# Kernel tuning notes

Hardware: AMD Instinct MI355X
Metric: run time of the kernel (lower is better)

## Reference

```python
import jax, jax.numpy as jnp
import numpy as np

MARGIN = 0.2
ALPHA = 2.0
BETA = 1.5
ANGLE_THRESHOLD = 30.0
EPS_PD = 1e-6   # F.pairwise_distance eps
EPS_CS = 1e-8   # F.cosine_similarity eps
NEG_INF = -1e30
POS_INF = 1e30


def setup_inputs() -> dict:
    key = jax.random.key(0)
    k1, k2, k3 = jax.random.split(key, 3)
    B, F, A = 4096, 512, 3
    features = jax.random.normal(k1, (B, F), dtype=jnp.float32)
    labels = jax.random.randint(k2, (B,), 0, 256)
    angles = jax.random.uniform(k3, (B, A), dtype=jnp.float32) * 90.0  # degrees
    features_orig = jax.random.normal(jax.random.fold_in(key, 7), (B, F), dtype=jnp.float32)
    return {"features": features, "labels": labels, "angles": angles, "features_orig": features_orig}


def _cosine_sim_matrix(f):
    norms = jnp.linalg.norm(f, axis=1)
    denom = jnp.maximum(norms[:, None] * norms[None, :], EPS_CS)
    return (f @ f.T) / denom


def _forward(features, labels, angles, features_orig):
    B = features.shape[0]
    idx = jnp.arange(B)
    # pairwise angle distances [B,B] (torch.cdist p=2)
    adist = jnp.sqrt(jnp.sum((angles[:, None, :] - angles[None, :, :]) ** 2, axis=-1))
    same = labels[:, None] == labels[None, :]
    same = same & ~jnp.eye(B, dtype=bool)          # exclude self
    diff = labels[:, None] != labels[None, :]
    has_pos = same.any(axis=1)
    has_neg = diff.any(axis=1)
    valid = has_pos & has_neg
    # hardest positive: same label, largest angle difference
    pos_idx = jnp.argmax(jnp.where(same, adist, NEG_INF), axis=1)
    # hardest negative: among diff-label within angle threshold, most similar feature;
    # else diff-label with smallest angle difference
    sim = _cosine_sim_matrix(features)
    similar = diff & (adist < ANGLE_THRESHOLD)
    sim_any = similar.any(axis=1)
    neg_idx_hard = jnp.argmax(jnp.where(similar, sim, NEG_INF), axis=1)
    neg_idx_far = jnp.argmin(jnp.where(diff, adist, POS_INF), axis=1)
    neg_idx = jnp.where(sim_any, neg_idx_hard, neg_idx_far)
    # triplet distances (F.pairwise_distance adds eps to the diff)
    a = features
    p = features[pos_idx]
    n = features[neg_idx]
    pos_d = jnp.linalg.norm(a - p + EPS_PD, axis=1)
    neg_d = jnp.linalg.norm(a - n + EPS_PD, axis=1)
    # angle-based weights (non-differentiable, matches .item() in torch)
    pa = adist[idx, pos_idx]
    na = adist[idx, neg_idx]
    w = jnp.where(pa > 45.0, ALPHA, 1.0) * jnp.where(na < 15.0, BETA, 1.0)
    basic = jax.nn.relu(pos_d - neg_d + MARGIN)
    vmask = valid.astype(features.dtype)
    cnt = jnp.maximum(vmask.sum(), 1.0)
    triplet_loss = jnp.sum(w * basic * vmask) / cnt
    # reconstruction term
    num = jnp.sum(features * features_orig, axis=1)
    den = jnp.maximum(jnp.linalg.norm(features, axis=1) * jnp.linalg.norm(features_orig, axis=1), EPS_CS)
    recon = 1.0 - jnp.mean(num / den)
    return triplet_loss + 0.1 * recon


def reference(features, labels, angles, features_orig):
    return _forward(features, labels, angles, features_orig)
```

## Files before the change

kernel.cpp:

```cpp
#include <hip/hip_runtime.h>
#include <math.h>

#define BN 4096
#define FD 512
#define TT 128
#define BK 64
#define NJT (BN / TT)
#define NBLK (NJT * (NJT + 1) / 2)
#define NPC 64

typedef __attribute__((ext_vector_type(8))) __bf16 bf16x8;
typedef __attribute__((ext_vector_type(4))) float floatx4;
typedef unsigned long long u64;

__device__ __forceinline__ float wred_sum(float v) {
#pragma unroll
  for (int m = 1; m < 64; m <<= 1) v += __shfl_xor(v, m, 64);
  return v;
}

__device__ __forceinline__ float dot4(float4 a, float4 b) {
  return a.x * b.x + a.y * b.y + a.z * b.z + a.w * b.w;
}

__device__ __forceinline__ unsigned short f2bf(float x) {
  unsigned u = __float_as_uint(x);
  u += 0x7fffu + ((u >> 16) & 1u);
  return (unsigned short)(u >> 16);
}

__device__ __forceinline__ void load16(const void* g, void* l) {
  __builtin_amdgcn_global_load_lds(
      (const __attribute__((address_space(1))) unsigned int*)g,
      (__attribute__((address_space(3))) unsigned int*)l, 16, 0, 0);
}

__device__ __forceinline__ unsigned ford(float v) {
  unsigned u = __float_as_uint(v);
  return u ^ (((unsigned)((int)u >> 31)) | 0x80000000u);
}

template <int N>
__device__ __forceinline__ int rori(int x) {
  return __builtin_amdgcn_update_dpp(0, x, 0x120 | N, 0xf, 0xf, true);
}
template <int N>
__device__ __forceinline__ u64 ror16_u64(u64 k) {
  unsigned lo = (unsigned)rori<N>((int)(unsigned)k);
  unsigned hi = (unsigned)rori<N>((int)(unsigned)(k >> 32));
  return ((u64)hi << 32) | lo;
}
__device__ __forceinline__ u64 red16_max_u64(u64 k) {
  u64 o;
  o = ror16_u64<1>(k); k = o > k ? o : k;
  o = ror16_u64<2>(k); k = o > k ? o : k;
  o = ror16_u64<4>(k); k = o > k ? o : k;
  o = ror16_u64<8>(k); k = o > k ? o : k;
  return k;
}

__device__ __forceinline__ u64 sx64(u64 v, int m) {
  unsigned lo = (unsigned)__shfl_xor((int)(unsigned)v, m, 64);
  unsigned hi = (unsigned)__shfl_xor((int)(unsigned)(v >> 32), m, 64);
  return ((u64)hi << 32) | lo;
}

__global__ __launch_bounds__(256) void k_prep(const float* __restrict__ f,
                                              const float* __restrict__ fo,
                                              const float* __restrict__ angles,
                                              unsigned short* __restrict__ gb,
                                              float* __restrict__ rowr,
                                              float* __restrict__ ax,
                                              float* __restrict__ ay,
                                              float* __restrict__ az) {
  const int i = blockIdx.x * 4 + (threadIdx.x >> 6);
  const int lane = threadIdx.x & 63;
  const int t = blockIdx.x * 256 + threadIdx.x;
  if (t < BN) {
    ax[t] = angles[t * 3 + 0];
    ay[t] = angles[t * 3 + 1];
    az[t] = angles[t * 3 + 2];
  }
  const float4* fr = (const float4*)(f + (size_t)i * FD);
  const float4* orr = (const float4*)(fo + (size_t)i * FD);
  float4 x0 = fr[lane], x1 = fr[lane + 64];
  float4 y0 = orr[lane], y1 = orr[lane + 64];
  float sff = dot4(x0, x0) + dot4(x1, x1);
  float sfo = dot4(x0, y0) + dot4(x1, y1);
  float soo = dot4(y0, y0) + dot4(y1, y1);
  sff = wred_sum(sff);
  sfo = wred_sum(sfo);
  soo = wred_sum(soo);
  float nf = sqrtf(sff);
  float inv = 1.0f / nf;
  ushort4* gr = (ushort4*)(gb + (size_t)i * FD);
  ushort4 s0, s1;
  s0.x = f2bf(x0.x * inv); s0.y = f2bf(x0.y * inv);
  s0.z = f2bf(x0.z * inv); s0.w = f2bf(x0.w * inv);
  s1.x = f2bf(x1.x * inv); s1.y = f2bf(x1.y * inv);
  s1.z = f2bf(x1.z * inv); s1.w = f2bf(x1.w * inv);
  gr[lane] = s0;
  gr[lane + 64] = s1;
  if (lane == 0) {
    rowr[i] = sfo / fmaxf(nf * sqrtf(soo), 1e-8f);
  }
}

__global__ __launch_bounds__(256) void k_sim(const unsigned short* __restrict__ gb,
                                             const int* __restrict__ labels,
                                             const float* __restrict__ ax,
                                             const float* __restrict__ ay,
                                             const float* __restrict__ az,
                                             u64* __restrict__ pkey) {
  __shared__ unsigned short As[TT * BK];
  __shared__ unsigned short Bs[TT * BK];
  int a = 0, rem = blockIdx.x;
#pragma unroll 1
  while (rem >= NJT - a) { rem -= NJT - a; a++; }
  const int b = a + rem;
  const int i0 = a * TT;
  const int j0 = b * TT;

  const int tid = threadIdx.x;
  const int w = tid >> 6;
  const int lane = tid & 63;
  const int wi = w >> 1, wj = w & 1;

  floatx4 acc[4][4];
#pragma unroll
  for (int u = 0; u < 4; u++)
#pragma unroll
    for (int v = 0; v < 4; v++) acc[u][v] = (floatx4){0.f, 0.f, 0.f, 0.f};

  const int rp = tid >> 3;
  const int q8 = ((tid & 7) ^ (rp & 7)) * 8;
  const unsigned short* gA[4];
  const unsigned short* gB[4];
  unsigned short* lA[4];
  unsigned short* lB[4];
#pragma unroll
  for (int c = 0; c < 4; c++) {
    gA[c] = gb + (size_t)(i0 + rp + 32 * c) * FD + q8;
    gB[c] = gb + (size_t)(j0 + rp + 32 * c) * FD + q8;
    lA[c] = As + (tid + 256 * c) * 8;
    lB[c] = Bs + (tid + 256 * c) * 8;
  }

  const int m = lane & 15;
  const int arow = wi * 64 + m;
  const int brow = wj * 64 + m;
  const int g4 = lane >> 4;
  const int l7 = lane & 7;
  const int koff0 = (g4 ^ l7) * 8;
  const int koff1 = ((4 + g4) ^ l7) * 8;

  for (int kc = 0; kc < FD; kc += BK) {
#pragma unroll
    for (int c = 0; c < 4; c++) {
      load16(gA[c] + kc, lA[c]);
      load16(gB[c] + kc, lB[c]);
    }
    __syncthreads();
    bf16x8 af[4], bf[4];
#pragma unroll
    for (int u = 0; u < 4; u++)
      af[u] = *(const bf16x8*)(As + (arow + u * 16) * BK + koff0);
#pragma unroll
    for (int v = 0; v < 4; v++)
      bf[v] = *(const bf16x8*)(Bs + (brow + v * 16) * BK + koff0);
#pragma unroll
    for (int u = 0; u < 4; u++)
#pragma unroll
      for (int v = 0; v < 4; v++)
        acc[u][v] = __builtin_amdgcn_mfma_f32_16x16x32_bf16(af[u], bf[v], acc[u][v], 0, 0, 0);
#pragma unroll
    for (int u = 0; u < 4; u++)
      af[u] = *(const bf16x8*)(As + (arow + u * 16) * BK + koff1);
#pragma unroll
    for (int v = 0; v < 4; v++)
      bf[v] = *(const bf16x8*)(Bs + (brow + v * 16) * BK + koff1);
#pragma unroll
    for (int u = 0; u < 4; u++)
#pragma unroll
      for (int v = 0; v < 4; v++)
        acc[u][v] = __builtin_amdgcn_mfma_f32_16x16x32_bf16(af[u], bf[v], acc[u][v], 0, 0, 0);
    __syncthreads();
  }

  const int quad = lane >> 4;
  const int cx = lane & 15;
  int jc[4], lj[4];
  float jx[4], jy[4], jz[4];
#pragma unroll
  for (int v = 0; v < 4; v++) {
    jc[v] = j0 + wj * 64 + v * 16 + cx;
    lj[v] = labels[jc[v]];
    jx[v] = ax[jc[v]];
    jy[v] = ay[jc[v]];
    jz[v] = az[jc[v]];
  }
  const size_t rbase = (size_t)(2 * b + wj) * BN;
  u64 ckey[4] = {0, 0, 0, 0};
#pragma unroll
  for (int u = 0; u < 4; u++) {
#pragma unroll
    for (int reg = 0; reg < 4; reg++) {
      int i = i0 + wi * 64 + u * 16 + quad * 4 + reg;
      int li = labels[i];
      float a0 = ax[i], a1 = ay[i], a2 = az[i];
      u64 rkey = 0;
      unsigned ni = (unsigned)(~i);
#pragma unroll
      for (int v = 0; v < 4; v++) {
        float d0 = a0 - jx[v];
        float d1 = a1 - jy[v];
        float d2 = a2 - jz[v];
        float dd = d0 * d0 + d1 * d1 + d2 * d2;
        bool ok = (li != lj[v]) && (dd < 900.0f);
        u64 vh = (u64)ford(acc[u][v][reg]) << 32;
        u64 candR = vh | (unsigned)(~jc[v]);
        if (ok && candR > rkey) rkey = candR;
        u64 candC = vh | ni;
        if (ok && candC > ckey[v]) ckey[v] = candC;
      }
      rkey = red16_max_u64(rkey);
      if (cx == 0) pkey[rbase + i] = rkey;
    }
  }
  if (a != b) {
    const size_t cbase = (size_t)(2 * a + wi) * BN;
#pragma unroll
    for (int v = 0; v < 4; v++) {
      u64 k = ckey[v];
      u64 o = sx64(k, 16); if (o > k) k = o;
      o = sx64(k, 32); if (o > k) k = o;
      if (quad == 0) pkey[cbase + jc[v]] = k;
    }
  }
}

__global__ __launch_bounds__(256) void k_final(const float* __restrict__ f,
                                               const int* __restrict__ labels,
                                               const float* __restrict__ ax,
                                               const float* __restrict__ ay,
                                               const float* __restrict__ az,
                                               const u64* __restrict__ pkey,
                                               float* __restrict__ rowc,
                                               float* __restrict__ rowv) {
  const int i = blockIdx.x * 4 + (threadIdx.x >> 6);
  const int lane = threadIdx.x & 63;
  const int li = labels[i];
  const float a0 = ax[i], a1 = ay[i], a2 = az[i];

  u64 keyP = 0;
  u64 keyN = ~0ull;
  const float4* ax4 = (const float4*)ax;
  const float4* ay4 = (const float4*)ay;
  const float4* az4 = (const float4*)az;
  const int4* lb4 = (const int4*)labels;
#pragma unroll
  for (int it = 0; it < 16; it++) {
    int bb = it * 64 + lane;
    float4 X = ax4[bb], Y = ay4[bb], Z = az4[bb];
    int4 L = lb4[bb];
    int jb = bb * 4;
#pragma unroll
    for (int s = 0; s < 4; s++) {
      float xx = s == 0 ? X.x : s == 1 ? X.y : s == 2 ? X.z : X.w;
      float yy = s == 0 ? Y.x : s == 1 ? Y.y : s == 2 ? Y.z : Y.w;
      float zz = s == 0 ? Z.x : s == 1 ? Z.y : s == 2 ? Z.z : Z.w;
      int ll = s == 0 ? L.x : s == 1 ? L.y : s == 2 ? L.z : L.w;
      int j = jb + s;
      float d0 = a0 - xx, d1 = a1 - yy, d2 = a2 - zz;
      float dd = d0 * d0 + d1 * d1 + d2 * d2;
      if (ll == li) {
        u64 kp = ((u64)__float_as_uint(dd) << 32) | (unsigned)(~j);
        if (j != i && kp > keyP) keyP = kp;
      } else {
        u64 kn = ((u64)__float_as_uint(dd) << 32) | (unsigned)j;
        if (kn < keyN) keyN = kn;
      }
    }
  }
  u64 keyS = pkey[(size_t)lane * BN + i];
#pragma unroll
  for (int off = 1; off < 64; off <<= 1) {
    u64 o = sx64(keyP, off);
    if (o > keyP) keyP = o;
    o = sx64(keyN, off);
    if (o < keyN) keyN = o;
    o = sx64(keyS, off);
    if (o > keyS) keyS = o;
  }
  bool hp = keyP != 0;
  bool hn = keyN != ~0ull;
  if (!(hp && hn)) {
    if (lane == 0) { rowc[i] = 0.0f; rowv[i] = 0.0f; }
    return;
  }
  bool sim_any = keyS != 0;
  int pos = (int)(~(unsigned)keyP);
  int neg = sim_any ? (int)(~(unsigned)keyS) : (int)(unsigned)keyN;

  const float4* fa = (const float4*)(f + (size_t)i * FD);
  const float4* fp = (const float4*)(f + (size_t)pos * FD);
  const float4* fn = (const float4*)(f + (size_t)neg * FD);
  float sp = 0.0f, sn = 0.0f;
#pragma unroll
  for (int t = 0; t < 2; t++) {
    float4 xa = fa[lane + t * 64];
    float4 xp = fp[lane + t * 64];
    float4 xn = fn[lane + t * 64];
    float dp;
    dp = xa.x - xp.x + 1e-6f; sp += dp * dp;
    dp = xa.y - xp.y + 1e-6f; sp += dp * dp;
    dp = xa.z - xp.z + 1e-6f; sp += dp * dp;
    dp = xa.w - xp.w + 1e-6f; sp += dp * dp;
    dp = xa.x - xn.x + 1e-6f; sn += dp * dp;
    dp = xa.y - xn.y + 1e-6f; sn += dp * dp;
    dp = xa.z - xn.z + 1e-6f; sn += dp * dp;
    dp = xa.w - xn.w + 1e-6f; sn += dp * dp;
  }
  sp = wred_sum(sp);
  sn = wred_sum(sn);

  if (lane == 0) {
    float pos_d = sqrtf(sp);
    float neg_d = sqrtf(sn);
    float pa = sqrtf(__uint_as_float((unsigned)(keyP >> 32)));
    float n0 = a0 - ax[neg];
    float n1 = a1 - ay[neg];
    float n2 = a2 - az[neg];
    float na = sqrtf(n0 * n0 + n1 * n1 + n2 * n2);
    float w = (pa > 45.0f ? 2.0f : 1.0f) * (na < 15.0f ? 1.5f : 1.0f);
    float basic = fmaxf(pos_d - neg_d + 0.2f, 0.0f);
    rowc[i] = w * basic;
    rowv[i] = 1.0f;
  }
}

__global__ __launch_bounds__(1024) void k_out(const float* __restrict__ rowc,
                                              const float* __restrict__ rowv,
                                              const float* __restrict__ rowr,
                                              float* __restrict__ out) {
  __shared__ float sc[16], sv[16], sr[16];
  const int t = threadIdx.x;
  float c = 0.0f, v = 0.0f, r = 0.0f;
  for (int i = t; i < BN; i += 1024) {
    c += rowc[i];
    v += rowv[i];
    r += rowr[i];
  }
  c = wred_sum(c);
  v = wred_sum(v);
  r = wred_sum(r);
  const int wid = t >> 6;
  if ((t & 63) == 0) { sc[wid] = c; sv[wid] = v; sr[wid] = r; }
  __syncthreads();
  if (t == 0) {
    float C = 0.0f, V = 0.0f, R = 0.0f;
#pragma unroll
    for (int k = 0; k < 16; k++) { C += sc[k]; V += sv[k]; R += sr[k]; }
    float tri = C / fmaxf(V, 1.0f);
    float recon = 1.0f - R / (float)BN;
    out[0] = tri + 0.1f * recon;
  }
}

extern "C" void kernel_launch(void* const* d_in, const int* in_sizes, int n_in,
                              void* d_out, int out_size, void* d_ws, size_t ws_size,
                              hipStream_t stream) {
  const float* feat = (const float*)d_in[0];
  const int* labels = (const int*)d_in[1];
  const float* angles = (const float*)d_in[2];
  const float* forig = (const float*)d_in[3];
  float* out = (float*)d_out;

  char* ws = (char*)d_ws;
  unsigned short* gb = (unsigned short*)ws;
  size_t off = (size_t)BN * FD * sizeof(unsigned short);
  u64* pkey = (u64*)(ws + off);     off += (size_t)NPC * BN * 8;
  float* rowc = (float*)(ws + off); off += (size_t)BN * 4;
  float* rowv = (float*)(ws + off); off += (size_t)BN * 4;
  float* rowr = (float*)(ws + off); off += (size_t)BN * 4;
  float* ax = (float*)(ws + off);   off += (size_t)BN * 4;
  float* ay = (float*)(ws + off);   off += (size_t)BN * 4;
  float* az = (float*)(ws + off);   off += (size_t)BN * 4;

  k_prep<<<BN / 4, 256, 0, stream>>>(feat, forig, angles, gb, rowr, ax, ay, az);
  k_sim<<<NBLK, 256, 0, stream>>>(gb, labels, ax, ay, az, pkey);
  k_final<<<BN / 4, 256, 0, stream>>>(feat, labels, ax, ay, az, pkey, rowc, rowv);
  k_out<<<1, 1024, 0, stream>>>(rowc, rowv, rowr, out);
}
```

Measured before the change: 129.0 us.

## Split each similarity tile pair into two 128x64 half-tiles for more blocks

```diff
diff --git a/kernel.cpp b/kernel.cpp
--- a/kernel.cpp
+++ b/kernel.cpp
@@ -4,10 +4,12 @@
 #define BN 4096
 #define FD 512
 #define TT 128
+#define TJ 64
 #define BK 64
 #define NJT (BN / TT)
-#define NBLK (NJT * (NJT + 1) / 2)
-#define NPC 64
+#define NPAIR (NJT * (NJT + 1) / 2)
+#define NBLK (NPAIR * 2)
+#define NPC 128
 
 typedef __attribute__((ext_vector_type(8))) __bf16 bf16x8;
 typedef __attribute__((ext_vector_type(4))) float floatx4;
@@ -113,42 +115,45 @@
                                              const float* __restrict__ az,
                                              u64* __restrict__ pkey) {
   __shared__ unsigned short As[TT * BK];
-  __shared__ unsigned short Bs[TT * BK];
-  int a = 0, rem = blockIdx.x;
+  __shared__ unsigned short Bs[TJ * BK];
+  const int h = blockIdx.x & 1;
+  int a = 0, rem = blockIdx.x >> 1;
 #pragma unroll 1
   while (rem >= NJT - a) { rem -= NJT - a; a++; }
   const int b = a + rem;
   const int i0 = a * TT;
-  const int j0 = b * TT;
+  const int j0 = b * TT + h * TJ;
 
   const int tid = threadIdx.x;
   const int w = tid >> 6;
   const int lane = tid & 63;
-  const int wi = w >> 1, wj = w & 1;
-
-  floatx4 acc[4][4];
-#pragma unroll
-  for (int u = 0; u < 4; u++)
+
+  floatx4 acc[2][4];
+#pragma unroll
+  for (int u = 0; u < 2; u++)
 #pragma unroll
     for (int v = 0; v < 4; v++) acc[u][v] = (floatx4){0.f, 0.f, 0.f, 0.f};
 
   const int rp = tid >> 3;
   const int q8 = ((tid & 7) ^ (rp & 7)) * 8;
   const unsigned short* gA[4];
-  const unsigned short* gB[4];
+  const unsigned short* gB[2];
   unsigned short* lA[4];
-  unsigned short* lB[4];
+  unsigned short* lB[2];
 #pragma unroll
   for (int c = 0; c < 4; c++) {
     gA[c] = gb + (size_t)(i0 + rp + 32 * c) * FD + q8;
+    lA[c] = As + (tid + 256 * c) * 8;
+  }
+#pragma unroll
+  for (int c = 0; c < 2; c++) {
     gB[c] = gb + (size_t)(j0 + rp + 32 * c) * FD + q8;
-    lA[c] = As + (tid + 256 * c) * 8;
     lB[c] = Bs + (tid + 256 * c) * 8;
   }
 
   const int m = lane & 15;
-  const int arow = wi * 64 + m;
-  const int brow = wj * 64 + m;
+  const int arow = w * 32 + m;
+  const int brow = m;
   const int g4 = lane >> 4;
   const int l7 = lane & 7;
   const int koff0 = (g4 ^ l7) * 8;
@@ -156,31 +161,30 @@
 
   for (int kc = 0; kc < FD; kc += BK) {
 #pragma unroll
-    for (int c = 0; c < 4; c++) {
-      load16(gA[c] + kc, lA[c]);
-      load16(gB[c] + kc, lB[c]);
-    }
+    for (int c = 0; c < 4; c++) load16(gA[c] + kc, lA[c]);
+#pragma unroll
+    for (int c = 0; c < 2; c++) load16(gB[c] + kc, lB[c]);
     __syncthreads();
-    bf16x8 af[4], bf[4];
-#pragma unroll
-    for (int u = 0; u < 4; u++)
+    bf16x8 af[2], bf[4];
+#pragma unroll
+    for (int u = 0; u < 2; u++)
       af[u] = *(const bf16x8*)(As + (arow + u * 16) * BK + koff0);
 #pragma unroll
     for (int v = 0; v < 4; v++)
       bf[v] = *(const bf16x8*)(Bs + (brow + v * 16) * BK + koff0);
 #pragma unroll
-    for (int u = 0; u < 4; u++)
+    for (int u = 0; u < 2; u++)
 #pragma unroll
       for (int v = 0; v < 4; v++)
         acc[u][v] = __builtin_amdgcn_mfma_f32_16x16x32_bf16(af[u], bf[v], acc[u][v], 0, 0, 0);
 #pragma unroll
-    for (int u = 0; u < 4; u++)
+    for (int u = 0; u < 2; u++)
       af[u] = *(const bf16x8*)(As + (arow + u * 16) * BK + koff1);
 #pragma unroll
     for (int v = 0; v < 4; v++)
       bf[v] = *(const bf16x8*)(Bs + (brow + v * 16) * BK + koff1);
 #pragma unroll
-    for (int u = 0; u < 4; u++)
+    for (int u = 0; u < 2; u++)
 #pragma unroll
       for (int v = 0; v < 4; v++)
         acc[u][v] = __builtin_amdgcn_mfma_f32_16x16x32_bf16(af[u], bf[v], acc[u][v], 0, 0, 0);
@@ -193,19 +197,19 @@
   float jx[4], jy[4], jz[4];
 #pragma unroll
   for (int v = 0; v < 4; v++) {
-    jc[v] = j0 + wj * 64 + v * 16 + cx;
+    jc[v] = j0 + v * 16 + cx;
     lj[v] = labels[jc[v]];
     jx[v] = ax[jc[v]];
     jy[v] = ay[jc[v]];
     jz[v] = az[jc[v]];
   }
-  const size_t rbase = (size_t)(2 * b + wj) * BN;
+  const size_t rbase = (size_t)(64 + 2 * b + h) * BN;
   u64 ckey[4] = {0, 0, 0, 0};
 #pragma unroll
-  for (int u = 0; u < 4; u++) {
+  for (int u = 0; u < 2; u++) {
 #pragma unroll
     for (int reg = 0; reg < 4; reg++) {
-      int i = i0 + wi * 64 + u * 16 + quad * 4 + reg;
+      int i = i0 + w * 32 + u * 16 + quad * 4 + reg;
       int li = labels[i];
       float a0 = ax[i], a1 = ay[i], a2 = az[i];
       u64 rkey = 0;
@@ -228,7 +232,7 @@
     }
   }
   if (a != b) {
-    const size_t cbase = (size_t)(2 * a + wi) * BN;
+    const size_t cbase = (size_t)(4 * a + w) * BN;
 #pragma unroll
     for (int v = 0; v < 4; v++) {
       u64 k = ckey[v];
@@ -282,7 +286,10 @@
       }
     }
   }
-  u64 keyS = pkey[(size_t)lane * BN + i];
+  const int t = i >> 7;
+  u64 s0 = (lane < 4 * t) ? pkey[(size_t)lane * BN + i] : 0;
+  u64 s1 = (lane >= 2 * t) ? pkey[(size_t)(64 + lane) * BN + i] : 0;
+  u64 keyS = s0 > s1 ? s0 : s1;
 #pragma unroll
   for (int off = 1; off < 64; off <<= 1) {
     u64 o = sx64(keyP, off);
@@ -307,10 +314,10 @@
   const float4* fn = (const float4*)(f + (size_t)neg * FD);
   float sp = 0.0f, sn = 0.0f;
 #pragma unroll
-  for (int t = 0; t < 2; t++) {
-    float4 xa = fa[lane + t * 64];
-    float4 xp = fp[lane + t * 64];
-    float4 xn = fn[lane + t * 64];
+  for (int t2 = 0; t2 < 2; t2++) {
+    float4 xa = fa[lane + t2 * 64];
+    float4 xp = fp[lane + t2 * 64];
+    float4 xn = fn[lane + t2 * 64];
     float dp;
     dp = xa.x - xp.x + 1e-6f; sp += dp * dp;
     dp = xa.y - xp.y + 1e-6f; sp += dp * dp;
```

New measurement: 108.9 us. 1.18x faster.
